# Optimization experiments

Hardware: AMD Instinct MI355X
Metric: run time of the kernel (lower is better)

The kernel has to match this reference:

```python
import jax, jax.numpy as jnp
import numpy as np

N, D_IN, D_LAT, D_FEAT, K = 12000, 64, 16, 64, 16


def setup_inputs() -> dict:
    key = jax.random.key(0)
    ks = jax.random.split(key, 7)
    s_in = 1.0 / np.sqrt(D_IN)
    s_cat = 1.0 / np.sqrt(2 * D_FEAT)
    return {
        "x": jax.random.normal(ks[0], (N, D_IN), dtype=jnp.float32),
        "W_feat": jax.random.uniform(ks[1], (D_IN, D_FEAT), jnp.float32, -s_in, s_in),
        "b_feat": jax.random.uniform(ks[2], (D_FEAT,), jnp.float32, -s_in, s_in),
        "W_lat": jax.random.uniform(ks[3], (D_IN, D_LAT), jnp.float32, -s_in, s_in),
        "b_lat": jax.random.uniform(ks[4], (D_LAT,), jnp.float32, -s_in, s_in),
        "W_out": jax.random.uniform(ks[5], (2 * D_FEAT, D_FEAT), jnp.float32, -s_cat, s_cat),
        "b_out": jax.random.uniform(ks[6], (D_FEAT,), jnp.float32, -s_cat, s_cat),
    }


def reference(x, W_feat, b_feat, W_lat, b_lat, W_out, b_out):
    # dense encoders
    feats = jnp.tanh(x @ W_feat + b_feat)      # [N, F] learned features
    coords = jnp.tanh(x @ W_lat + b_lat)       # [N, S] latent coordinates
    n = coords.shape[0]
    # full pairwise squared euclidean distances (as the module's cdist)
    sq = jnp.sum(coords * coords, axis=1)
    d2 = sq[:, None] + sq[None, :] - 2.0 * (coords @ coords.T)   # [N, N]
    d2 = jnp.maximum(d2, 0.0)
    # knn_graph: k nearest neighbors, excluding self (loop=False)
    d2_masked = jnp.where(jnp.eye(n, dtype=bool), jnp.inf, d2)
    neg_d2, idx = jax.lax.top_k(-d2_masked, K)                   # idx: [N, K] neighbor (source) ids
    edge_d2 = -neg_d2                                            # squared dist to each neighbor
    # gaussian kernel on euclidean distance: w = exp(-d^2)
    w = jnp.exp(-edge_d2)                                        # [N, K]
    # message = w * x_j, aggr='add': out_i = sum_k w_ik * feats[idx_ik]
    agg = jnp.einsum('nk,nkf->nf', w, feats[idx])                # [N, F]
    # cat self features with aggregated messages, final dense
    out = jnp.concatenate([feats, agg], axis=1) @ W_out + b_out  # [N, F]
    return out
```

## Files before the change

### kernel.cpp

```cpp
#include <hip/hip_runtime.h>
#include <math.h>

typedef unsigned long long u64;
typedef _Float16 f16x8 __attribute__((ext_vector_type(8)));
typedef float f32x16 __attribute__((ext_vector_type(16)));

#define N_PTS 12000
#define KNN 16
#define QB 16
#define NWAVES 8
#define NGROUPS32 (N_PTS / 32)
#define TAU_PTS 2048
#define TAU_GROUPS32 (TAU_PTS / 32)
#define CAP 384
#define MARGIN 0.08f

__global__ __launch_bounds__(256) void encoder_kernel(
    const float* __restrict__ x, const float* __restrict__ Wf, const float* __restrict__ bf,
    const float* __restrict__ Wl, const float* __restrict__ bl,
    float* __restrict__ feats, float* __restrict__ coords, _Float16* __restrict__ coords_h,
    float* __restrict__ sq)
{
  const int wave = threadIdx.x >> 6;
  const int lane = threadIdx.x & 63;
  const int i = blockIdx.x * 4 + wave;
  if (i >= N_PTS) return;
  float xv = x[i * 64 + lane];
  float accf = bf[lane];
  float accc = bl[lane & 15];
  #pragma unroll
  for (int k = 0; k < 64; ++k) {
    float xk = __shfl(xv, k);
    accf = fmaf(xk, Wf[k * 64 + lane], accf);
    accc = fmaf(xk, Wl[k * 16 + (lane & 15)], accc);
  }
  feats[i * 64 + lane] = tanhf(accf);
  float c = tanhf(accc);
  float cc = (lane < 16) ? c * c : 0.0f;
  cc += __shfl_xor(cc, 1);
  cc += __shfl_xor(cc, 2);
  cc += __shfl_xor(cc, 4);
  cc += __shfl_xor(cc, 8);
  if (lane < 16) {
    coords[i * 16 + lane] = c;
    coords_h[i * 16 + lane] = (_Float16)c;
  }
  if (lane == 0) sq[i] = cc;
}

__device__ __forceinline__ void ins6(u64 key, u64* k6, u64& kmax) {
  const u64 om = (key < kmax) ? kmax : ~0ull;
  #pragma unroll
  for (int t = 0; t < 6; ++t)
    k6[t] = (k6[t] == om) ? key : k6[t];
  u64 a = k6[0] > k6[1] ? k6[0] : k6[1];
  u64 b = k6[2] > k6[3] ? k6[2] : k6[3];
  u64 c = k6[4] > k6[5] ? k6[4] : k6[5];
  a = a > b ? a : b;
  kmax = a > c ? a : c;
}

__device__ __forceinline__ void ins8(u64 key, u64* k8, u64& kmax) {
  const u64 om = (key < kmax) ? kmax : ~0ull;
  #pragma unroll
  for (int t = 0; t < 8; ++t)
    k8[t] = (k8[t] == om) ? key : k8[t];
  u64 a = k8[0] > k8[1] ? k8[0] : k8[1];
  u64 b = k8[2] > k8[3] ? k8[2] : k8[3];
  u64 c = k8[4] > k8[5] ? k8[4] : k8[5];
  u64 d = k8[6] > k8[7] ? k8[6] : k8[7];
  a = a > b ? a : b;
  c = c > d ? c : d;
  kmax = a > c ? a : c;
}

__device__ __forceinline__ u64 shflx_u64(u64 v, int off) {
  int lo = __shfl_xor((int)(unsigned)v, off);
  int hi = __shfl_xor((int)(unsigned)(v >> 32), off);
  return ((u64)(unsigned)hi << 32) | (unsigned)lo;
}

__device__ __forceinline__ u64 minbfly(u64 m) {
  #pragma unroll
  for (int off = 32; off >= 1; off >>= 1) {
    u64 o = shflx_u64(m, off);
    m = (o < m) ? o : m;
  }
  return m;
}

__global__ __launch_bounds__(512) void knn_agg_kernel(
    const float* __restrict__ coords, const _Float16* __restrict__ coords_h,
    const float* __restrict__ sq, const float* __restrict__ feats,
    const float* __restrict__ Wo, const float* __restrict__ bo,
    float* __restrict__ out, int* __restrict__ flags)
{
  __shared__ unsigned short sbuf[QB][CAP];
  __shared__ int scnt[QB];
  __shared__ unsigned colminS[QB][64];
  __shared__ float taugS[QB];
  __shared__ float featS[QB][64];
  __shared__ float aggS[QB][64];

  const int tid = threadIdx.x;
  const int lane = tid & 63;
  const int wave = tid >> 6;
  const int qbase = blockIdx.x * QB;
  const int mcol = lane & 31;
  const int half = lane >> 5;

  if (tid < QB) scnt[tid] = 0;
  #pragma unroll
  for (int t = tid; t < QB * 64; t += 512)
    ((unsigned*)colminS)[t] = 0x7F800000u;

  f16x8 afrag = {0, 0, 0, 0, 0, 0, 0, 0};
  if (mcol < QB) {
    const uint4 u = *(const uint4*)((const char*)coords_h + (qbase + mcol) * 32 + half * 16);
    afrag = __builtin_bit_cast(f16x8, u);
  }
  float sqi8[8];
  #pragma unroll
  for (int blk = 0; blk < 2; ++blk) {
    const float4 v = *(const float4*)&sq[qbase + blk * 8 + 4 * half];
    sqi8[blk * 4 + 0] = v.x; sqi8[blk * 4 + 1] = v.y;
    sqi8[blk * 4 + 2] = v.z; sqi8[blk * 4 + 3] = v.w;
  }
  __syncthreads();

  float lmin8[8] = {INFINITY, INFINITY, INFINITY, INFINITY,
                    INFINITY, INFINITY, INFINITY, INFINITY};
  for (int g = wave; g < TAU_GROUPS32; g += NWAVES) {
    const int j0 = g * 32;
    const uint4 u = *(const uint4*)((const char*)coords_h + (j0 + mcol) * 32 + half * 16);
    const f16x8 bfrag = __builtin_bit_cast(f16x8, u);
    const float sqj = sq[j0 + mcol];
    f32x16 acc = {0.0f};
    acc = __builtin_amdgcn_mfma_f32_32x32x16_f16(afrag, bfrag, acc, 0, 0, 0);
    #pragma unroll
    for (int r = 0; r < 8; ++r) {
      const int row = (r >> 2) * 8 + 4 * half + (r & 3);
      float d2a = fmaf(-2.0f, acc[r], sqi8[r] + sqj);
      if (j0 + mcol == qbase + row) d2a = INFINITY;
      lmin8[r] = fminf(lmin8[r], d2a);
    }
  }
  {
    const int cell = mcol * 2 + (wave >> 2);
    #pragma unroll
    for (int r = 0; r < 8; ++r) {
      const int row = (r >> 2) * 8 + 4 * half + (r & 3);
      atomicMin(&colminS[row][cell], __float_as_uint(fmaxf(lmin8[r], 0.0f)));
    }
  }
  __syncthreads();

  #pragma unroll
  for (int s = 0; s < 2; ++s) {
    const int q = wave * 2 + s;
    float v = __uint_as_float(colminS[q][lane]);
    #pragma unroll
    for (int k = 2; k <= 64; k <<= 1) {
      #pragma unroll
      for (int st = k >> 1; st >= 1; st >>= 1) {
        const float o = __shfl_xor(v, st);
        const bool keepMin = (((lane & st) == 0) == ((lane & k) == 0));
        const float mn = fminf(v, o), mx = fmaxf(v, o);
        v = keepMin ? mn : mx;
      }
    }
    const float tq = __shfl(v, 15) + MARGIN;
    if (lane == 0) taugS[q] = tq;
  }
  __syncthreads();

  float taug8[8];
  #pragma unroll
  for (int r = 0; r < 8; ++r)
    taug8[r] = taugS[(r >> 2) * 8 + 4 * half + (r & 3)];

  for (int g = wave; g < NGROUPS32; g += NWAVES) {
    const int j0 = g * 32;
    const uint4 u = *(const uint4*)((const char*)coords_h + (j0 + mcol) * 32 + half * 16);
    const f16x8 bfrag = __builtin_bit_cast(f16x8, u);
    const float sqj = sq[j0 + mcol];
    f32x16 acc = {0.0f};
    acc = __builtin_amdgcn_mfma_f32_32x32x16_f16(afrag, bfrag, acc, 0, 0, 0);
    #pragma unroll
    for (int r = 0; r < 8; ++r) {
      const float d2a = fmaf(-2.0f, acc[r], sqi8[r] + sqj);
      if (d2a <= taug8[r]) {
        const int row = (r >> 2) * 8 + 4 * half + (r & 3);
        const int p = atomicAdd(&scnt[row], 1);
        if (p < CAP) sbuf[row][p] = (unsigned short)(j0 + mcol);
      }
    }
  }
  __syncthreads();

  #pragma unroll
  for (int s = 0; s < 2; ++s) {
    const int lq = wave * 2 + s;
    const int qg = qbase + lq;
    const int cq = scnt[lq];
    const int nread = (cq < CAP) ? cq : CAP;

    float ci[16];
    {
      const float4* cp = (const float4*)(coords + qg * 16);
      *(float4*)&ci[0] = cp[0]; *(float4*)&ci[4] = cp[1];
      *(float4*)&ci[8] = cp[2]; *(float4*)&ci[12] = cp[3];
    }
    const float sqiq = sq[qg];

    u64 k6[6];
    #pragma unroll
    for (int t = 0; t < 6; ++t) k6[t] = ((u64)(0x7F000000u + t) << 32);
    u64 kmax6 = ((u64)0x7F000005u << 32);

    #pragma unroll
    for (int t = 0; t < CAP / 64; ++t) {
      const int idx = t * 64 + lane;
      u64 key = ~0ull;
      if (idx < nread) {
        const int jj = sbuf[lq][idx];
        if (jj != qg) {
          const float4* cp = (const float4*)(coords + jj * 16);
          float cj[16];
          *(float4*)&cj[0]  = cp[0]; *(float4*)&cj[4]  = cp[1];
          *(float4*)&cj[8]  = cp[2]; *(float4*)&cj[12] = cp[3];
          float dot = 0.0f;
          #pragma unroll
          for (int d = 0; d < 16; ++d) dot = fmaf(ci[d], cj[d], dot);
          const float d2 = fmaxf(fmaf(-2.0f, dot, sqiq + sq[jj]), 0.0f);
          key = ((u64)__float_as_uint(d2) << 32) | (unsigned)jj;
        }
      }
      ins6(key, k6, kmax6);
    }

    u64 lmin = k6[0];
    #pragma unroll
    for (int t = 1; t < 6; ++t) lmin = (k6[t] < lmin) ? k6[t] : lmin;

    float aggv = 0.0f;
    for (int r = 0; r < KNN; ++r) {
      const u64 m = minbfly(lmin);
      if (lmin == m) {
        #pragma unroll
        for (int t = 0; t < 6; ++t) k6[t] = (k6[t] == m) ? ~0ull : k6[t];
        lmin = k6[0];
        #pragma unroll
        for (int t = 1; t < 6; ++t) lmin = (k6[t] < lmin) ? k6[t] : lmin;
      }
      const unsigned hi = (unsigned)(m >> 32);
      const bool ok = hi < 0x7F000000u;
      const float w = ok ? expf(-__uint_as_float(hi)) : 0.0f;
      const int jj = ok ? (int)(unsigned)(m & 0xFFFFFFFFull) : 0;
      aggv = fmaf(w, feats[jj * 64 + lane], aggv);
    }
    aggS[lq][lane] = aggv;
    featS[lq][lane] = feats[qg * 64 + lane];
    if (lane == 0) flags[qg] = (cq > CAP);
  }

  __syncthreads();
  const int row = tid >> 5;
  const int c0 = tid & 31;
  float acc0 = bo[c0], acc1 = bo[c0 + 32];
  #pragma unroll
  for (int f = 0; f < 64; ++f) {
    const float fv = featS[row][f];
    const float av = aggS[row][f];
    acc0 = fmaf(fv, Wo[f * 64 + c0],        acc0);
    acc1 = fmaf(fv, Wo[f * 64 + c0 + 32],   acc1);
    acc0 = fmaf(av, Wo[(64 + f) * 64 + c0],      acc0);
    acc1 = fmaf(av, Wo[(64 + f) * 64 + c0 + 32], acc1);
  }
  const int orow = qbase + row;
  out[orow * 64 + c0]      = acc0;
  out[orow * 64 + c0 + 32] = acc1;
}

__global__ __launch_bounds__(256) void knn_fixup_kernel(
    const float* __restrict__ coords, const float* __restrict__ sq,
    const float* __restrict__ feats, const int* __restrict__ flags,
    const float* __restrict__ Wo, const float* __restrict__ bo,
    float* __restrict__ out)
{
  const int wave = threadIdx.x >> 6;
  const int lane = threadIdx.x & 63;
  const int i = blockIdx.x * 4 + wave;
  if (i >= N_PTS) return;
  if (!flags[i]) return;
  float ci[16];
  #pragma unroll
  for (int d = 0; d < 16; ++d) ci[d] = coords[i * 16 + d];
  const float sqi = sq[i];

  u64 k8a[8], k8b[8], kmaxA, kmaxB;
  #pragma unroll
  for (int t = 0; t < 8; ++t) {
    k8a[t] = ((u64)(0x7F000000u + t) << 32);
    k8b[t] = ((u64)(0x7F000000u + t) << 32);
  }
  kmaxA = ((u64)0x7F000007u << 32);
  kmaxB = ((u64)0x7F000007u << 32);

  const int niter = (N_PTS + 63) / 64;
  for (int t = 0; t < niter; ++t) {
    const int j = t * 64 + lane;
    float4 c0 = make_float4(0,0,0,0), c1 = c0, c2 = c0, c3 = c0;
    float sqj = 0.0f;
    if (j < N_PTS) {
      const float4* cp = (const float4*)(coords + j * 16);
      c0 = cp[0]; c1 = cp[1]; c2 = cp[2]; c3 = cp[3];
      sqj = sq[j];
    }
    float dot = ci[0]*c0.x + ci[1]*c0.y + ci[2]*c0.z + ci[3]*c0.w
              + ci[4]*c1.x + ci[5]*c1.y + ci[6]*c1.z + ci[7]*c1.w
              + ci[8]*c2.x + ci[9]*c2.y + ci[10]*c2.z + ci[11]*c2.w
              + ci[12]*c3.x + ci[13]*c3.y + ci[14]*c3.z + ci[15]*c3.w;
    float d2 = fmaxf(fmaf(-2.0f, dot, sqi + sqj), 0.0f);
    const unsigned hi = (j == i || j >= N_PTS) ? 0xFFFFFFFFu : __float_as_uint(d2);
    const u64 key = ((u64)hi << 32) | (unsigned)j;
    if (t & 1) ins8(key, k8a, kmaxA);
    else       ins8(key, k8b, kmaxB);
  }

  u64 tab[16];
  #pragma unroll
  for (int t = 0; t < 8; ++t) { tab[t] = k8a[t]; tab[8 + t] = k8b[t]; }
  u64 lmin = tab[0];
  #pragma unroll
  for (int t = 1; t < 16; ++t) lmin = (tab[t] < lmin) ? tab[t] : lmin;

  float aggv = 0.0f;
  u64 T16 = 0;
  for (int r = 0; r < KNN; ++r) {
    const u64 m = minbfly(lmin);
    if (lmin == m) {
      #pragma unroll
      for (int t = 0; t < 16; ++t) tab[t] = (tab[t] == m) ? ~0ull : tab[t];
      lmin = tab[0];
      #pragma unroll
      for (int t = 1; t < 16; ++t) lmin = (tab[t] < lmin) ? tab[t] : lmin;
    }
    const unsigned hi = (unsigned)(m >> 32);
    const bool ok = hi < 0x7F000000u;
    const float w = ok ? expf(-__uint_as_float(hi)) : 0.0f;
    const int jj = ok ? (int)(unsigned)(m & 0xFFFFFFFFull) : 0;
    aggv = fmaf(w, feats[jj * 64 + lane], aggv);
    T16 = m;
  }

  if (__any((kmaxA < T16) || (kmaxB < T16))) {
    aggv = 0.0f;
    u64 prev = 0;
    for (int r = 0; r < KNN; ++r) {
      u64 best = ~0ull;
      for (int j = lane; j < N_PTS; j += 64) {
        float dot = 0.0f;
        #pragma unroll
        for (int d = 0; d < 16; ++d) dot = fmaf(ci[d], coords[j * 16 + d], dot);
        const float d2 = fmaxf(fmaf(-2.0f, dot, sqi + sq[j]), 0.0f);
        const unsigned hi = (j == i) ? 0xFFFFFFFFu : __float_as_uint(d2);
        const u64 key = ((u64)hi << 32) | (unsigned)j;
        const bool cand = (r == 0) || (key > prev);
        if (cand && key < best) best = key;
      }
      const u64 m = minbfly(best);
      prev = m;
      const unsigned hi = (unsigned)(m >> 32);
      const bool ok = hi < 0x7F000000u;
      const float w = ok ? expf(-__uint_as_float(hi)) : 0.0f;
      const int jj = ok ? (int)(unsigned)(m & 0xFFFFFFFFull) : 0;
      aggv = fmaf(w, feats[jj * 64 + lane], aggv);
    }
  }

  const float fl = feats[i * 64 + lane];
  float acc = bo[lane];
  #pragma unroll
  for (int f = 0; f < 64; ++f) {
    acc = fmaf(__shfl(fl, f),   Wo[f * 64 + lane],        acc);
    acc = fmaf(__shfl(aggv, f), Wo[(64 + f) * 64 + lane], acc);
  }
  out[i * 64 + lane] = acc;
}

extern "C" void kernel_launch(void* const* d_in, const int* in_sizes, int n_in,
                              void* d_out, int out_size, void* d_ws, size_t ws_size,
                              hipStream_t stream) {
  const float* x  = (const float*)d_in[0];
  const float* Wf = (const float*)d_in[1];
  const float* bf = (const float*)d_in[2];
  const float* Wl = (const float*)d_in[3];
  const float* bl = (const float*)d_in[4];
  const float* Wo = (const float*)d_in[5];
  const float* bo = (const float*)d_in[6];
  float* out = (float*)d_out;

  char* ws = (char*)d_ws;
  float*     feats    = (float*)(ws);
  float*     coords   = (float*)(ws + 3072000);
  float*     sqv      = (float*)(ws + 3840000);
  _Float16*  coords_h = (_Float16*)(ws + 3888000);
  int*       flags    = (int*)(ws + 4272000);

  encoder_kernel<<<3000, 256, 0, stream>>>(x, Wf, bf, Wl, bl, feats, coords, coords_h, sqv);
  knn_agg_kernel<<<N_PTS / QB, 512, 0, stream>>>(coords, coords_h, sqv, feats, Wo, bo, out, flags);
  knn_fixup_kernel<<<3000, 256, 0, stream>>>(coords, sqv, feats, flags, Wo, bo, out);
}
```

Baseline: 174.0 us.

## Simplify candidate filter, bound refine loop, decouple top-k extraction, vectorize output

```diff
diff --git a/kernel.cpp b/kernel.cpp
--- a/kernel.cpp
+++ b/kernel.cpp
@@ -14,6 +14,7 @@
 #define TAU_GROUPS32 (TAU_PTS / 32)
 #define CAP 384
 #define MARGIN 0.08f
+#define EVICT_KEY ((u64)0x7F400000u << 32)
 
 __global__ __launch_bounds__(256) void encoder_kernel(
     const float* __restrict__ x, const float* __restrict__ Wf, const float* __restrict__ bf,
@@ -174,22 +175,21 @@
   }
   __syncthreads();
 
-  float taug8[8];
+  float thr8[8];
   #pragma unroll
   for (int r = 0; r < 8; ++r)
-    taug8[r] = taugS[(r >> 2) * 8 + 4 * half + (r & 3)];
+    thr8[r] = 0.5f * (sqi8[r] - taugS[(r >> 2) * 8 + 4 * half + (r & 3)]);
 
   for (int g = wave; g < NGROUPS32; g += NWAVES) {
     const int j0 = g * 32;
     const uint4 u = *(const uint4*)((const char*)coords_h + (j0 + mcol) * 32 + half * 16);
     const f16x8 bfrag = __builtin_bit_cast(f16x8, u);
-    const float sqj = sq[j0 + mcol];
+    const float hs = 0.5f * sq[j0 + mcol];
     f32x16 acc = {0.0f};
     acc = __builtin_amdgcn_mfma_f32_32x32x16_f16(afrag, bfrag, acc, 0, 0, 0);
     #pragma unroll
     for (int r = 0; r < 8; ++r) {
-      const float d2a = fmaf(-2.0f, acc[r], sqi8[r] + sqj);
-      if (d2a <= taug8[r]) {
+      if (acc[r] >= thr8[r] + hs) {
         const int row = (r >> 2) * 8 + 4 * half + (r & 3);
         const int p = atomicAdd(&scnt[row], 1);
         if (p < CAP) sbuf[row][p] = (unsigned short)(j0 + mcol);
@@ -204,6 +204,7 @@
     const int qg = qbase + lq;
     const int cq = scnt[lq];
     const int nread = (cq < CAP) ? cq : CAP;
+    const int nit = (nread + 63) >> 6;
 
     float ci[16];
     {
@@ -218,8 +219,7 @@
     for (int t = 0; t < 6; ++t) k6[t] = ((u64)(0x7F000000u + t) << 32);
     u64 kmax6 = ((u64)0x7F000005u << 32);
 
-    #pragma unroll
-    for (int t = 0; t < CAP / 64; ++t) {
+    for (int t = 0; t < nit; ++t) {
       const int idx = t * 64 + lane;
       u64 key = ~0ull;
       if (idx < nread) {
@@ -242,23 +242,37 @@
     u64 lmin = k6[0];
     #pragma unroll
     for (int t = 1; t < 6; ++t) lmin = (k6[t] < lmin) ? k6[t] : lmin;
-
-    float aggv = 0.0f;
+    float dmin = __uint_as_float((unsigned)(lmin >> 32));
+    int jmin = (int)(unsigned)(lmin & 0xFFFFFFFFull);
+
+    float dv[16]; int jv[16];
+    #pragma unroll
     for (int r = 0; r < KNN; ++r) {
-      const u64 m = minbfly(lmin);
-      if (lmin == m) {
+      float m = dmin;
+      #pragma unroll
+      for (int off = 32; off >= 1; off >>= 1)
+        m = fminf(m, __shfl_xor(m, off));
+      const u64 bal = __ballot(dmin == m);
+      const int owner = __ffsll((unsigned long long)bal) - 1;
+      jv[r] = __builtin_amdgcn_readlane(jmin, owner);
+      dv[r] = __uint_as_float(__builtin_amdgcn_readfirstlane(__float_as_uint(m)));
+      if (lane == owner) {
         #pragma unroll
-        for (int t = 0; t < 6; ++t) k6[t] = (k6[t] == m) ? ~0ull : k6[t];
+        for (int t = 0; t < 6; ++t)
+          k6[t] = (k6[t] == lmin) ? EVICT_KEY : k6[t];
         lmin = k6[0];
         #pragma unroll
         for (int t = 1; t < 6; ++t) lmin = (k6[t] < lmin) ? k6[t] : lmin;
+        dmin = __uint_as_float((unsigned)(lmin >> 32));
+        jmin = (int)(unsigned)(lmin & 0xFFFFFFFFull);
       }
-      const unsigned hi = (unsigned)(m >> 32);
-      const bool ok = hi < 0x7F000000u;
-      const float w = ok ? expf(-__uint_as_float(hi)) : 0.0f;
-      const int jj = ok ? (int)(unsigned)(m & 0xFFFFFFFFull) : 0;
-      aggv = fmaf(w, feats[jj * 64 + lane], aggv);
-    }
+    }
+
+    float aggv = 0.0f;
+    #pragma unroll
+    for (int r = 0; r < KNN; ++r)
+      aggv = fmaf(expf(-dv[r]), feats[jv[r] * 64 + lane], aggv);
+
     aggS[lq][lane] = aggv;
     featS[lq][lane] = feats[qg * 64 + lane];
     if (lane == 0) flags[qg] = (cq > CAP);
@@ -266,20 +280,19 @@
 
   __syncthreads();
   const int row = tid >> 5;
-  const int c0 = tid & 31;
-  float acc0 = bo[c0], acc1 = bo[c0 + 32];
+  const int c2 = (tid & 31) * 2;
+  float acc0 = bo[c2], acc1 = bo[c2 + 1];
   #pragma unroll
   for (int f = 0; f < 64; ++f) {
     const float fv = featS[row][f];
     const float av = aggS[row][f];
-    acc0 = fmaf(fv, Wo[f * 64 + c0],        acc0);
-    acc1 = fmaf(fv, Wo[f * 64 + c0 + 32],   acc1);
-    acc0 = fmaf(av, Wo[(64 + f) * 64 + c0],      acc0);
-    acc1 = fmaf(av, Wo[(64 + f) * 64 + c0 + 32], acc1);
+    const float2 w0 = *(const float2*)&Wo[f * 64 + c2];
+    const float2 w1 = *(const float2*)&Wo[(64 + f) * 64 + c2];
+    acc0 = fmaf(fv, w0.x, acc0); acc0 = fmaf(av, w1.x, acc0);
+    acc1 = fmaf(fv, w0.y, acc1); acc1 = fmaf(av, w1.y, acc1);
   }
   const int orow = qbase + row;
-  out[orow * 64 + c0]      = acc0;
-  out[orow * 64 + c0 + 32] = acc1;
+  *(float2*)&out[orow * 64 + c2] = make_float2(acc0, acc1);
 }
 
 __global__ __launch_bounds__(256) void knn_fixup_kernel(
```

Measured after the change: 172.0 us. No clear change (-1.2%).
